# Kernel tuning notes

Hardware: AMD Instinct MI355X
Metric: run time of the kernel (lower is better)

## Reference

```python
import jax, jax.numpy as jnp
import numpy as np


def _gru_scan(xg, w_hh, b_hh, h0):
    """Scan a GRU (PyTorch gate order r,z,n) over time. xg: (T,B,3H) precomputed input projections."""
    def step(h, g):
        gh = h @ w_hh.T + b_hh
        i_r, i_z, i_n = jnp.split(g, 3, axis=-1)
        h_r, h_z, h_n = jnp.split(gh, 3, axis=-1)
        r = jax.nn.sigmoid(i_r + h_r)
        z = jax.nn.sigmoid(i_z + h_z)
        n = jnp.tanh(i_n + r * h_n)
        h_new = (1.0 - z) * n + z * h
        return h_new, h_new
    _, ys = jax.lax.scan(step, h0, xg)
    return ys  # (T, B, H)


def setup_inputs() -> dict:
    key = jax.random.key(0)
    ks = jax.random.split(key, 13)
    B, M, T = 64, 80, 2000
    C, H, K = 256, 256, 5
    s = 0.1
    return {
        "x": jax.random.normal(ks[0], (B, M, T), jnp.float32),
        "conv_w": jax.random.normal(ks[1], (C, M, K), jnp.float32) * s,
        "conv_b": jax.random.normal(ks[2], (C,), jnp.float32) * s,
        "w_ih_f": jax.random.normal(ks[3], (3 * H, C), jnp.float32) * s,
        "w_hh_f": jax.random.normal(ks[4], (3 * H, H), jnp.float32) * s,
        "b_ih_f": jax.random.normal(ks[5], (3 * H,), jnp.float32) * s,
        "b_hh_f": jax.random.normal(ks[6], (3 * H,), jnp.float32) * s,
        "w_ih_r": jax.random.normal(ks[7], (3 * H, C), jnp.float32) * s,
        "w_hh_r": jax.random.normal(ks[8], (3 * H, H), jnp.float32) * s,
        "b_ih_r": jax.random.normal(ks[9], (3 * H,), jnp.float32) * s,
        "b_hh_r": jax.random.normal(ks[10], (3 * H,), jnp.float32) * s,
        "clf_w": jax.random.normal(ks[11], (2, 2 * H), jnp.float32) * s,
        "clf_b": jax.random.normal(ks[12], (2,), jnp.float32) * s,
        "window_size": 100,
    }


def reference(x, conv_w, conv_b, w_ih_f, w_hh_f, b_ih_f, b_hh_f,
              w_ih_r, w_hh_r, b_ih_r, b_hh_r, clf_w, clf_b, window_size):
    # Streaming (inference_mode) branch of KWSNet, expressed incrementally:
    # per-step sliding-window conv == full valid conv; the 'bidirectional' GRU
    # with seq_len=1 per step and carried hidden == two independent GRUs both
    # scanned forward in time (one with the _reverse weight set).
    B = x.shape[0]
    K = conv_w.shape[-1]
    H = w_hh_f.shape[-1]
    # Conv1d valid + ReLU: (B, C, Tc), Tc = T - K + 1
    y = jax.lax.conv_general_dilated(x, conv_w, (1,), 'VALID',
                                     dimension_numbers=('NCH', 'OIH', 'NCH'))
    y = jax.nn.relu(y + conv_b[None, :, None])
    seq = jnp.transpose(y, (2, 0, 1))  # (Tc, B, C)
    h0 = jnp.zeros((B, H), seq.dtype)
    xg_f = seq @ w_ih_f.T + b_ih_f  # (Tc, B, 3H)
    xg_r = seq @ w_ih_r.T + b_ih_r
    enc = jnp.concatenate([
        _gru_scan(xg_f, w_hh_f, b_hh_f, h0),
        _gru_scan(xg_r, w_hh_r, b_hh_r, h0),
    ], axis=-1)  # (Tc, B, 2H)
    # Sliding mean over the last W encoder outputs (W = window_size - K + 1)
    W = window_size - K + 1
    cs = jnp.concatenate([jnp.zeros_like(enc[:1]), jnp.cumsum(enc, axis=0)], axis=0)
    means = (cs[W:] - cs[:-W]) / W  # (Tout, B, 2H), Tout = T - window_size + 1
    out = means @ clf_w.T + clf_b  # (Tout, B, 2)
    # torch stacks per-step (1, B, 2) outputs -> (Tout, 1, B, 2)
    return out[:, None, :, :]
```

## Files before the change

kernel.cpp:

```cpp
#include <hip/hip_runtime.h>
#include <hip/hip_bf16.h>


#define TT    2000
#define TC    1996
#define NB    64
#define MCH   80
#define NH    256
#define NN    1536
#define TOUT  1901
#define TCH   250
#define NCHK  8
#define CROWS (TCH * NB)

typedef _Float16 h2_t __attribute__((ext_vector_type(2)));
typedef _Float16 h8_t __attribute__((ext_vector_type(8)));
typedef float    f4_t __attribute__((ext_vector_type(4)));

#define WQSCALE 254.0f
#define INV8    (1.0f / (254.0f * 127.0f))

#define OFF_SEQC ((size_t)0)
#define OFF_XG   ((size_t)8192000)
#define OFF_WT   ((size_t)57344000)
#define OFF_WCAT ((size_t)57753600)
#define OFF_PSUM ((size_t)58540032)
#define OFF_HST  ((size_t)59561984)
#define OFF_WQ   ((size_t)59693056)
#define OFF_ENC  ((size_t)60086272)

__global__ void prep_kernel(const float* __restrict__ conv_w,
                            const float* __restrict__ wihf,
                            const float* __restrict__ wihr,
                            const float* __restrict__ whhf,
                            const float* __restrict__ whhr,
                            float* __restrict__ wT,
                            _Float16* __restrict__ wcat,
                            unsigned* __restrict__ wq) {
    int idx = blockIdx.x * 256 + threadIdx.x;
    if (idx < 400 * 256) {
        int c = idx & 255, mk = idx >> 8;
        wT[idx] = conv_w[c * 400 + mk];
    }
    int i2 = idx - 400 * 256;
    if (i2 >= 0 && i2 < NN * 256) {
        int k = i2 & 255, n = i2 >> 8;
        float v = (n < 768) ? wihf[n * 256 + k] : wihr[(n - 768) * 256 + k];
        wcat[i2] = (_Float16)v;
    }
    int i4 = idx - (400 * 256 + NN * 256);
    if (i4 >= 0 && i4 < 2 * 3 * 256 * 64) {
        int r  = i4 & 255;
        int j  = (i4 >> 8) & 63;
        int dg = i4 >> 14;
        const float* whh = (dg >= 3) ? whhr : whhf;
        int g = (dg >= 3) ? dg - 3 : dg;
        const float* wp = whh + (size_t)(g * 256 + r) * 256 + 4 * j;
        unsigned v = 0;
#pragma unroll
        for (int kk = 0; kk < 4; ++kk) {
            float q = rintf(wp[kk] * WQSCALE);
            q = fminf(fmaxf(q, -127.f), 127.f);
            v |= ((unsigned)((int)q & 0xFF)) << (8 * kk);
        }
        wq[((size_t)dg * 256 + r) * 64 + j] = v;
    }
}

__global__ __launch_bounds__(256, 2)
void conv_kernel(const float* __restrict__ x, const float* __restrict__ wT,
                 const float* __restrict__ conv_b, _Float16* __restrict__ seqc,
                 int t_base, int t_len) {
    __shared__ float xs[MCH][68];
    int tile = blockIdx.x;
    int b    = blockIdx.y;
    int tid  = threadIdx.x;
    for (int idx = tid; idx < MCH * 68; idx += 256) {
        int m = idx / 68, i = idx - m * 68;
        int tt = t_base + tile * 64 + i;
        xs[m][i] = (tt < TT) ? x[(size_t)b * (MCH * TT) + m * TT + tt] : 0.f;
    }
    __syncthreads();
    int lane = tid & 63, tg = tid >> 6;
    float acc[4][16];
#pragma unroll
    for (int cq = 0; cq < 4; ++cq)
#pragma unroll
        for (int t = 0; t < 16; ++t) acc[cq][t] = 0.f;

    for (int m = 0; m < MCH; ++m) {
        float xr_[20];
#pragma unroll
        for (int q = 0; q < 5; ++q) {
            float4 v = *(const float4*)&xs[m][tg * 16 + q * 4];
            xr_[q * 4 + 0] = v.x; xr_[q * 4 + 1] = v.y;
            xr_[q * 4 + 2] = v.z; xr_[q * 4 + 3] = v.w;
        }
#pragma unroll
        for (int cq = 0; cq < 4; ++cq) {
            int c = lane + cq * 64;
            const float* wp = wT + (size_t)(m * 5) * 256 + c;
            float w0_ = wp[0], w1_ = wp[256], w2_ = wp[512], w3_ = wp[768], w4_ = wp[1024];
#pragma unroll
            for (int t = 0; t < 16; ++t)
                acc[cq][t] += w0_ * xr_[t] + w1_ * xr_[t + 1] + w2_ * xr_[t + 2]
                            + w3_ * xr_[t + 3] + w4_ * xr_[t + 4];
        }
    }
#pragma unroll
    for (int cq = 0; cq < 4; ++cq) {
        int c = lane + cq * 64;
        float cb = conv_b[c];
        for (int t = 0; t < 16; ++t) {
            int tl = tile * 64 + tg * 16 + t;
            if (tl < t_len) {
                float v = acc[cq][t] + cb;
                v = v > 0.f ? v : 0.f;
                seqc[((size_t)tl * 64 + b) * 256 + c] = (_Float16)v;
            }
        }
    }
}

__global__ __launch_bounds__(256, 2)
void proj_kernel(const _Float16* __restrict__ seqc, const _Float16* __restrict__ wcat,
                 const float* __restrict__ bihf, const float* __restrict__ bihr,
                 _Float16* __restrict__ xg) {
    __shared__ __align__(16) _Float16 As[128][72];
    __shared__ __align__(16) _Float16 Bs[128][72];
    int row0 = blockIdx.x * 128;
    int n0   = blockIdx.y * 128;
    int tid  = threadIdx.x;
    int lane = tid & 63, wv = tid >> 6;
    int wr = wv >> 1, wc = wv & 1;
    int fm = lane & 15, fq = lane >> 4;
    f4_t acc[4][4];
#pragma unroll
    for (int mt = 0; mt < 4; ++mt)
#pragma unroll
        for (int nt = 0; nt < 4; ++nt) acc[mt][nt] = (f4_t){0.f, 0.f, 0.f, 0.f};

    int r = tid >> 1, part = tid & 1;
    for (int kc = 0; kc < 4; ++kc) {
        const uint4* srcA = (const uint4*)&seqc[(size_t)(row0 + r) * 256 + kc * 64 + part * 32];
        const uint4* srcB = (const uint4*)&wcat[(size_t)(n0 + r) * 256 + kc * 64 + part * 32];
        uint4* dstA = (uint4*)&As[r][part * 32];
        uint4* dstB = (uint4*)&Bs[r][part * 32];
        dstA[0] = srcA[0]; dstA[1] = srcA[1]; dstA[2] = srcA[2]; dstA[3] = srcA[3];
        dstB[0] = srcB[0]; dstB[1] = srcB[1]; dstB[2] = srcB[2]; dstB[3] = srcB[3];
        __syncthreads();
#pragma unroll
        for (int ks = 0; ks < 64; ks += 32) {
            h8_t af[4], bf[4];
#pragma unroll
            for (int mt = 0; mt < 4; ++mt)
                af[mt] = *(const h8_t*)&As[wr * 64 + mt * 16 + fm][ks + fq * 8];
#pragma unroll
            for (int nt = 0; nt < 4; ++nt)
                bf[nt] = *(const h8_t*)&Bs[wc * 64 + nt * 16 + fm][ks + fq * 8];
#pragma unroll
            for (int mt = 0; mt < 4; ++mt)
#pragma unroll
                for (int nt = 0; nt < 4; ++nt)
                    acc[mt][nt] = __builtin_amdgcn_mfma_f32_16x16x32_f16(
                        af[mt], bf[nt], acc[mt][nt], 0, 0, 0);
        }
        __syncthreads();
    }
#pragma unroll
    for (int nt = 0; nt < 4; ++nt) {
        int col = n0 + wc * 64 + nt * 16 + fm;
        int d = (col < 768) ? 0 : 1;
        int j = col - d * 768;
        float bias = d ? bihr[j] : bihf[j];
        size_t obase = (size_t)d * CROWS * 768 + j;
#pragma unroll
        for (int mt = 0; mt < 4; ++mt) {
            int row = row0 + wr * 64 + mt * 16 + fq * 4;
#pragma unroll
            for (int rr = 0; rr < 4; ++rr)
                xg[obase + (size_t)(row + rr) * 768] = (_Float16)(acc[mt][nt][rr] + bias);
        }
    }
}

#define SD4(a, b, c) __builtin_amdgcn_sdot4((int)(a), (int)(b), (c), false)

__global__ __launch_bounds__(256)
void scan_kernel(const _Float16* __restrict__ xg, const uint4* __restrict__ wq,
                 const float* __restrict__ bhhf, const float* __restrict__ bhhr,
                 float* __restrict__ hstate, _Float16* __restrict__ encc,
                 int t0, int len, int first) {
    int blk = blockIdx.x;
    int d = blk >> 6, b = blk & 63;
    int i = threadIdx.x;
    const float* bhh = d ? bhhr : bhhf;

    __shared__ __align__(16) unsigned hq8[2][64];

    uint4 wa[16], wb[16], wc[16];
    {
        const uint4* pa = wq + ((size_t)(d * 3 + 0) * 256 + i) * 16;
        const uint4* pb = wq + ((size_t)(d * 3 + 1) * 256 + i) * 16;
        const uint4* pc = wq + ((size_t)(d * 3 + 2) * 256 + i) * 16;
#pragma unroll
        for (int k = 0; k < 16; ++k) { wa[k] = pa[k]; wb[k] = pb[k]; wc[k] = pc[k]; }
    }
    float bhr = bhh[i], bhz = bhh[256 + i], bhn = bhh[512 + i];
    float h = first ? 0.f : hstate[(size_t)blk * 256 + i];

    ((char*)&hq8[0][0])[i] = (char)(int)rintf(h * 127.f);
    __syncthreads();

    const _Float16* xgp = xg + (size_t)d * CROWS * 768 + (size_t)b * 768 + i;
    float xr = (float)xgp[0], xz = (float)xgp[256], xn = (float)xgp[512];
    xgp += (size_t)64 * 768;
    _Float16* ep = encc + (size_t)b * 512 + d * 256 + i;

    int cur = 0;
    for (int t = 0; t < len; ++t) {
        float pxr = (float)xgp[0], pxz = (float)xgp[256], pxn = (float)xgp[512];
        xgp += (size_t)64 * 768;

        const uint4* hqp = (const uint4*)&hq8[cur][0];
        int i0 = 0, i1 = 0, i2 = 0;
#pragma unroll
        for (int k = 0; k < 16; ++k) {
            uint4 hv = hqp[k];
            i0 = SD4(wa[k].x, hv.x, i0); i0 = SD4(wa[k].y, hv.y, i0);
            i0 = SD4(wa[k].z, hv.z, i0); i0 = SD4(wa[k].w, hv.w, i0);
            i1 = SD4(wb[k].x, hv.x, i1); i1 = SD4(wb[k].y, hv.y, i1);
            i1 = SD4(wb[k].z, hv.z, i1); i1 = SD4(wb[k].w, hv.w, i1);
            i2 = SD4(wc[k].x, hv.x, i2); i2 = SD4(wc[k].y, hv.y, i2);
            i2 = SD4(wc[k].z, hv.z, i2); i2 = SD4(wc[k].w, hv.w, i2);
        }

        float hr = (float)i0 * INV8 + bhr;
        float hz = (float)i1 * INV8 + bhz;
        float hn = (float)i2 * INV8 + bhn;
        float rg = 1.f / (1.f + __expf(-(xr + hr)));
        float zg = 1.f / (1.f + __expf(-(xz + hz)));
        float xnr = xn + rg * hn;
        float nv = 1.f - 2.f / (__expf(2.f * xnr) + 1.f);
        h = (1.f - zg) * nv + zg * h;

        int nxt = cur ^ 1;
        ((char*)&hq8[nxt][0])[i] = (char)(int)rintf(h * 127.f);
        ep[(size_t)t * 64 * 512] = (_Float16)h;
        __syncthreads();
        cur = nxt;
        xr = pxr; xz = pxz; xn = pxn;
    }
    hstate[(size_t)blk * 256 + i] = h;
}

__global__ __launch_bounds__(256)
void clf_kernel(const _Float16* __restrict__ encc, const float* __restrict__ clf_w,
                float* __restrict__ psum, int t0, int len) {
    int w = (blockIdx.x * 256 + threadIdx.x) >> 6;
    int lane = threadIdx.x & 63;
    if (w >= len * 64) return;
    const _Float16* row = encc + (size_t)w * 512 + lane * 8;
    uint4 v = *(const uint4*)row;
    float4 c0a = *(const float4*)(clf_w + lane * 8);
    float4 c0b = *(const float4*)(clf_w + lane * 8 + 4);
    float4 c1a = *(const float4*)(clf_w + 512 + lane * 8);
    float4 c1b = *(const float4*)(clf_w + 512 + lane * 8 + 4);
    h2_t e0 = __builtin_bit_cast(h2_t, v.x), e1 = __builtin_bit_cast(h2_t, v.y);
    h2_t e2 = __builtin_bit_cast(h2_t, v.z), e3 = __builtin_bit_cast(h2_t, v.w);
    float s0 = c0a.x * (float)e0[0] + c0a.y * (float)e0[1] + c0a.z * (float)e1[0] + c0a.w * (float)e1[1]
             + c0b.x * (float)e2[0] + c0b.y * (float)e2[1] + c0b.z * (float)e3[0] + c0b.w * (float)e3[1];
    float s1 = c1a.x * (float)e0[0] + c1a.y * (float)e0[1] + c1a.z * (float)e1[0] + c1a.w * (float)e1[1]
             + c1b.x * (float)e2[0] + c1b.y * (float)e2[1] + c1b.z * (float)e3[0] + c1b.w * (float)e3[1];
#pragma unroll
    for (int off = 32; off; off >>= 1) {
        s0 += __shfl_xor(s0, off, 64);
        s1 += __shfl_xor(s1, off, 64);
    }
    if (lane == 0) {
        int tl = w >> 6, b = w & 63;
        psum[((size_t)(t0 + tl) * 64 + b) * 2 + 0] = s0;
        psum[((size_t)(t0 + tl) * 64 + b) * 2 + 1] = s1;
    }
}

__global__ void final_kernel(const float* __restrict__ psum, const float* __restrict__ clf_b,
                             const int* __restrict__ win, float* __restrict__ out) {
    int idx = blockIdx.x * 256 + threadIdx.x;
    if (idx >= TOUT * 128) return;
    int c = idx & 1;
    int rem = idx >> 1;
    int b = rem & 63;
    int tau = rem >> 6;
    int W = win[0] - 5 + 1;
    float s = 0.f;
    for (int j = 0; j < W; ++j)
        s += psum[((size_t)(tau + j) * 64 + b) * 2 + c];
    out[idx] = s / (float)W + clf_b[c];
}

extern "C" void kernel_launch(void* const* d_in, const int* in_sizes, int n_in,
                              void* d_out, int out_size, void* d_ws, size_t ws_size,
                              hipStream_t stream) {
    const float* x      = (const float*)d_in[0];
    const float* conv_w = (const float*)d_in[1];
    const float* conv_b = (const float*)d_in[2];
    const float* w_ih_f = (const float*)d_in[3];
    const float* w_hh_f = (const float*)d_in[4];
    const float* b_ih_f = (const float*)d_in[5];
    const float* b_hh_f = (const float*)d_in[6];
    const float* w_ih_r = (const float*)d_in[7];
    const float* w_hh_r = (const float*)d_in[8];
    const float* b_ih_r = (const float*)d_in[9];
    const float* b_hh_r = (const float*)d_in[10];
    const float* clf_w  = (const float*)d_in[11];
    const float* clf_b  = (const float*)d_in[12];
    const int*   win    = (const int*)d_in[13];
    float* out = (float*)d_out;

    char* ws = (char*)d_ws;
    _Float16* seqc = (_Float16*)(ws + OFF_SEQC);
    _Float16* xg   = (_Float16*)(ws + OFF_XG);
    float*    wT   = (float*)(ws + OFF_WT);
    _Float16* wcat = (_Float16*)(ws + OFF_WCAT);
    float*    psum = (float*)(ws + OFF_PSUM);
    float*    hst  = (float*)(ws + OFF_HST);
    unsigned* wq   = (unsigned*)(ws + OFF_WQ);
    _Float16* encc = (_Float16*)(ws + OFF_ENC);

    int prep_elems = 400 * 256 + NN * 256 + 2 * 3 * 256 * 64;
    prep_kernel<<<(prep_elems + 255) / 256, 256, 0, stream>>>(
        conv_w, w_ih_f, w_ih_r, w_hh_f, w_hh_r, wT, wcat, wq);

    for (int c = 0; c < NCHK; ++c) {
        int t0  = c * TCH;
        int len = (c == NCHK - 1) ? (TC - t0) : TCH;
        conv_kernel<<<dim3(4, 64), 256, 0, stream>>>(x, wT, conv_b, seqc, t0, len);
        proj_kernel<<<dim3(len * 64 / 128, 12), 256, 0, stream>>>(seqc, wcat, b_ih_f, b_ih_r, xg);
        scan_kernel<<<128, 256, 0, stream>>>(xg, (const uint4*)wq, b_hh_f, b_hh_r,
                                             hst, encc, t0, len, c == 0);
        clf_kernel<<<len * 16, 256, 0, stream>>>(encc, clf_w, psum, t0, len);
    }
    final_kernel<<<(TOUT * 128 + 255) / 256, 256, 0, stream>>>(psum, clf_b, win, out);
}
```

Before: 2.489 ms.

## Split GRU recurrent dot product across two thread halves with readlane broadcast

```diff
diff --git a/kernel.cpp b/kernel.cpp
--- a/kernel.cpp
+++ b/kernel.cpp
@@ -185,73 +185,87 @@
 }
 
 #define SD4(a, b, c) __builtin_amdgcn_sdot4((int)(a), (int)(b), (c), false)
-
-__global__ __launch_bounds__(256)
+#define RL(v, l)     __builtin_amdgcn_readlane((int)(v), (l))
+
+#define HCHUNK(k)                                                              \
+    int hx##k = RL(blob.x, k), hy##k = RL(blob.y, k),                          \
+        hz##k = RL(blob.z, k), hw##k = RL(blob.w, k);                          \
+    i0 = SD4(wa[k].x, hx##k, i0); i0 = SD4(wa[k].y, hy##k, i0);                \
+    i0 = SD4(wa[k].z, hz##k, i0); i0 = SD4(wa[k].w, hw##k, i0);                \
+    i1 = SD4(wb[k].x, hx##k, i1); i1 = SD4(wb[k].y, hy##k, i1);                \
+    i1 = SD4(wb[k].z, hz##k, i1); i1 = SD4(wb[k].w, hw##k, i1);                \
+    i2 = SD4(wc[k].x, hx##k, i2); i2 = SD4(wc[k].y, hy##k, i2);                \
+    i2 = SD4(wc[k].z, hz##k, i2); i2 = SD4(wc[k].w, hw##k, i2);
+
+__global__ __launch_bounds__(512)
 void scan_kernel(const _Float16* __restrict__ xg, const uint4* __restrict__ wq,
                  const float* __restrict__ bhhf, const float* __restrict__ bhhr,
                  float* __restrict__ hstate, _Float16* __restrict__ encc,
                  int t0, int len, int first) {
     int blk = blockIdx.x;
     int d = blk >> 6, b = blk & 63;
-    int i = threadIdx.x;
+    int tid = threadIdx.x;
+    int i = tid & 255, half = tid >> 8;
+    int lane = tid & 63;
     const float* bhh = d ? bhhr : bhhf;
 
     __shared__ __align__(16) unsigned hq8[2][64];
-
-    uint4 wa[16], wb[16], wc[16];
+    __shared__ int parr[3][256];
+
+    uint4 wa[8], wb[8], wc[8];
     {
-        const uint4* pa = wq + ((size_t)(d * 3 + 0) * 256 + i) * 16;
-        const uint4* pb = wq + ((size_t)(d * 3 + 1) * 256 + i) * 16;
-        const uint4* pc = wq + ((size_t)(d * 3 + 2) * 256 + i) * 16;
-#pragma unroll
-        for (int k = 0; k < 16; ++k) { wa[k] = pa[k]; wb[k] = pb[k]; wc[k] = pc[k]; }
-    }
-    float bhr = bhh[i], bhz = bhh[256 + i], bhn = bhh[512 + i];
-    float h = first ? 0.f : hstate[(size_t)blk * 256 + i];
-
-    ((char*)&hq8[0][0])[i] = (char)(int)rintf(h * 127.f);
+        const uint4* pa = wq + ((size_t)(d * 3 + 0) * 256 + i) * 16 + half * 8;
+        const uint4* pb = wq + ((size_t)(d * 3 + 1) * 256 + i) * 16 + half * 8;
+        const uint4* pc = wq + ((size_t)(d * 3 + 2) * 256 + i) * 16 + half * 8;
+#pragma unroll
+        for (int k = 0; k < 8; ++k) { wa[k] = pa[k]; wb[k] = pb[k]; wc[k] = pc[k]; }
+    }
+    float bhr = 0.f, bhz = 0.f, bhn = 0.f, h = 0.f;
+    if (half == 0) {
+        bhr = bhh[i]; bhz = bhh[256 + i]; bhn = bhh[512 + i];
+        h = first ? 0.f : hstate[(size_t)blk * 256 + i];
+        ((char*)&hq8[0][0])[i] = (char)(int)rintf(h * 127.f);
+    }
     __syncthreads();
 
     const _Float16* xgp = xg + (size_t)d * CROWS * 768 + (size_t)b * 768 + i;
-    float xr = (float)xgp[0], xz = (float)xgp[256], xn = (float)xgp[512];
+    float xr = 0.f, xz = 0.f, xn = 0.f;
+    if (half == 0) { xr = (float)xgp[0]; xz = (float)xgp[256]; xn = (float)xgp[512]; }
     xgp += (size_t)64 * 768;
     _Float16* ep = encc + (size_t)b * 512 + d * 256 + i;
 
     int cur = 0;
     for (int t = 0; t < len; ++t) {
-        float pxr = (float)xgp[0], pxz = (float)xgp[256], pxn = (float)xgp[512];
+        float pxr = 0.f, pxz = 0.f, pxn = 0.f;
+        if (half == 0) { pxr = (float)xgp[0]; pxz = (float)xgp[256]; pxn = (float)xgp[512]; }
         xgp += (size_t)64 * 768;
 
-        const uint4* hqp = (const uint4*)&hq8[cur][0];
+        uint4 blob = *((const uint4*)&hq8[cur][half * 32] + (lane & 7));
         int i0 = 0, i1 = 0, i2 = 0;
-#pragma unroll
-        for (int k = 0; k < 16; ++k) {
-            uint4 hv = hqp[k];
-            i0 = SD4(wa[k].x, hv.x, i0); i0 = SD4(wa[k].y, hv.y, i0);
-            i0 = SD4(wa[k].z, hv.z, i0); i0 = SD4(wa[k].w, hv.w, i0);
-            i1 = SD4(wb[k].x, hv.x, i1); i1 = SD4(wb[k].y, hv.y, i1);
-            i1 = SD4(wb[k].z, hv.z, i1); i1 = SD4(wb[k].w, hv.w, i1);
-            i2 = SD4(wc[k].x, hv.x, i2); i2 = SD4(wc[k].y, hv.y, i2);
-            i2 = SD4(wc[k].z, hv.z, i2); i2 = SD4(wc[k].w, hv.w, i2);
-        }
-
-        float hr = (float)i0 * INV8 + bhr;
-        float hz = (float)i1 * INV8 + bhz;
-        float hn = (float)i2 * INV8 + bhn;
-        float rg = 1.f / (1.f + __expf(-(xr + hr)));
-        float zg = 1.f / (1.f + __expf(-(xz + hz)));
-        float xnr = xn + rg * hn;
-        float nv = 1.f - 2.f / (__expf(2.f * xnr) + 1.f);
-        h = (1.f - zg) * nv + zg * h;
-
-        int nxt = cur ^ 1;
-        ((char*)&hq8[nxt][0])[i] = (char)(int)rintf(h * 127.f);
-        ep[(size_t)t * 64 * 512] = (_Float16)h;
+        HCHUNK(0) HCHUNK(1) HCHUNK(2) HCHUNK(3)
+        HCHUNK(4) HCHUNK(5) HCHUNK(6) HCHUNK(7)
+
+        if (half == 1) {
+            parr[0][i] = i0; parr[1][i] = i1; parr[2][i] = i2;
+        }
         __syncthreads();
-        cur = nxt;
+        if (half == 0) {
+            float hr = (float)(i0 + parr[0][i]) * INV8 + bhr;
+            float hz = (float)(i1 + parr[1][i]) * INV8 + bhz;
+            float hn = (float)(i2 + parr[2][i]) * INV8 + bhn;
+            float rg = 1.f / (1.f + __expf(-(xr + hr)));
+            float zg = 1.f / (1.f + __expf(-(xz + hz)));
+            float xnr = xn + rg * hn;
+            float nv = 1.f - 2.f / (__expf(2.f * xnr) + 1.f);
+            h = (1.f - zg) * nv + zg * h;
+            ((char*)&hq8[cur ^ 1][0])[i] = (char)(int)rintf(h * 127.f);
+            ep[(size_t)t * 64 * 512] = (_Float16)h;
+        }
+        __syncthreads();
+        cur ^= 1;
         xr = pxr; xz = pxz; xn = pxn;
     }
-    hstate[(size_t)blk * 256 + i] = h;
+    if (half == 0) hstate[(size_t)blk * 256 + i] = h;
 }
 
 __global__ __launch_bounds__(256)
@@ -337,7 +351,7 @@
         int len = (c == NCHK - 1) ? (TC - t0) : TCH;
         conv_kernel<<<dim3(4, 64), 256, 0, stream>>>(x, wT, conv_b, seqc, t0, len);
         proj_kernel<<<dim3(len * 64 / 128, 12), 256, 0, stream>>>(seqc, wcat, b_ih_f, b_ih_r, xg);
-        scan_kernel<<<128, 256, 0, stream>>>(xg, (const uint4*)wq, b_hh_f, b_hh_r,
+        scan_kernel<<<128, 512, 0, stream>>>(xg, (const uint4*)wq, b_hh_f, b_hh_r,
                                              hst, encc, t0, len, c == 0);
         clf_kernel<<<len * 16, 256, 0, stream>>>(encc, clf_w, psum, t0, len);
     }
```

Result: slower. 2.841 ms (+14.2%).
